# Kernel tuning notes

Measured on AMD Instinct MI355X. Metric: run time of the kernel, lower is better.

## Reference

```python
import jax, jax.numpy as jnp
from jax import lax
import numpy as np

EPS = 1e-5

def _conv(x, w, b, pad, dil=1):
    y = lax.conv_general_dilated(x, w, (1, 1), [(pad, pad), (pad, pad)],
                                 rhs_dilation=(dil, dil),
                                 dimension_numbers=('NCHW', 'OIHW', 'NCHW'))
    return y + b[None, :, None, None]

def _bn(x, g, b):
    # BatchNorm2d in training mode: batch stats over (N,H,W)
    m = x.mean((0, 2, 3), keepdims=True)
    v = x.var((0, 2, 3), keepdims=True)
    return (x - m) * lax.rsqrt(v + EPS) * g[None, :, None, None] + b[None, :, None, None]

def _median_filter(x, k=5):
    # faithful to source: 5x5 box SUM of reflect-padded shifts, then median over channels
    p = k // 2
    xp = jnp.pad(x, ((0, 0), (0, 0), (p, p), (p, p)), mode='reflect')
    s = lax.reduce_window(xp, 0.0, lax.add, (1, 1, k, k), (1, 1, 1, 1), 'VALID')
    return jnp.median(s, axis=1, keepdims=True)

def _idwt2_haar(ca, ch, cv, cd):
    # pywt.idwt2 haar convention: cH = row-detail ('da'), cV = col-detail ('ad')
    B, C, H, W = ca.shape
    y00 = (ca + ch + cv + cd) * 0.5
    y01 = (ca + ch - cv - cd) * 0.5
    y10 = (ca - ch + cv - cd) * 0.5
    y11 = (ca - ch - cv + cd) * 0.5
    even = jnp.stack([y00, y01], axis=-1).reshape(B, C, H, 2 * W)
    odd = jnp.stack([y10, y11], axis=-1).reshape(B, C, H, 2 * W)
    return jnp.stack([even, odd], axis=-2).reshape(B, C, 2 * H, 2 * W)

def _forward(ll_freq, hl_freq, lh_freq, hh_freq, w_ll, w_hl, w_lh, w_hh,
             cc_w, cc_b, bnc_g, bnc_b, e1_w, e1_b, fe_w, fe_b, e2_w, e2_b,
             bne_g, bne_b, cr_w, cr_b, bnr_g, bnr_b,
             adj_w, adj_b, cll_w, cll_b, chh_w, chh_b,
             c1_w, c1_b, c3_w, c3_b, c5_w, c5_b):
    C = hh_freq.shape[1]
    ll = w_ll * ll_freq
    hl = w_hl * hl_freq
    lh = w_lh * lh_freq
    hh = w_hh * hh_freq
    hh_m = jnp.tile(_median_filter(hh), (1, C, 1, 1))
    hh_l1 = hh_m + hh_freq
    # CCFEA SE-style block on concat(hl, lh)
    x = jnp.concatenate([hl, lh], axis=1)
    orig = x
    x = _conv(x, cc_w, cc_b, 0)
    x = _conv(x, e1_w, e1_b, 1)
    x = jax.nn.relu(_bn(x, bnc_g, bnc_b))
    x = _conv(x, fe_w, fe_b, 0)
    x = _conv(x, e2_w, e2_b, 2)
    x = jax.nn.relu(_bn(x, bne_g, bne_b))
    x = _conv(x, cr_w, cr_b, 0)
    x = _bn(x, bnr_g, bnr_b)
    x = orig * jax.nn.sigmoid(x)
    hl_l1, lh_l1 = jnp.split(x, 2, axis=1)
    # multi-kernel LL branch
    ll_l1 = _conv(ll, c1_w, c1_b, 1)
    ll_l1 = _conv(ll_l1, c3_w, c3_b, 2)
    ll_l1 = _conv(ll_l1, c5_w, c5_b, 3)
    ll_l2 = _conv(jnp.concatenate([ll_l1, ll], axis=1), adj_w, adj_b, 0)
    hl_l2 = _conv(jnp.concatenate([hl_l1, hl_freq], axis=1), adj_w, adj_b, 0)
    lh_l2 = _conv(jnp.concatenate([lh_l1, lh_freq], axis=1), adj_w, adj_b, 0)
    hh_a = jax.nn.leaky_relu(_conv(hh_l1, chh_w, chh_b, 0), 0.1)
    hh_l2 = jnp.tanh(_conv(hh_a, cll_w, cll_b, 4, dil=2))  # k=5, dilation=2, pad=4 -> same size
    return _idwt2_haar(ll_l2, hl_l2, lh_l2, hh_l2)

def setup_inputs() -> dict:
    key = jax.random.key(0)
    ks = jax.random.split(key, 16)
    B, C, H, W = 8, 64, 64, 64
    RED, EXP = 16, 8 * C  # reduction_ratio=16, expanded = (2C)*4 = 512
    f32 = jnp.float32
    def w(k, shape, s=0.05):
        return jax.random.normal(k, shape, dtype=f32) * s
    z = lambda n: jnp.zeros((n,), f32)
    o = lambda n: jnp.ones((n,), f32)
    return {
        'll_freq': jax.random.normal(ks[0], (B, C, H, W), dtype=f32),
        'hl_freq': jax.random.normal(ks[1], (B, C, H, W), dtype=f32),
        'lh_freq': jax.random.normal(ks[2], (B, C, H, W), dtype=f32),
        'hh_freq': jax.random.normal(ks[3], (B, C, H, W), dtype=f32),
        'w_ll': jnp.asarray(1.0, f32), 'w_hl': jnp.asarray(1.0, f32),
        'w_lh': jnp.asarray(1.0, f32), 'w_hh': jnp.asarray(1.0, f32),
        'cc_w': w(ks[4], (RED, 2 * C, 1, 1)), 'cc_b': z(RED),
        'bnc_g': o(RED), 'bnc_b': z(RED),
        'e1_w': w(ks[5], (RED, RED, 3, 3)), 'e1_b': z(RED),
        'fe_w': w(ks[6], (EXP, RED, 1, 1)), 'fe_b': z(EXP),
        'e2_w': w(ks[7], (EXP, EXP, 5, 5)), 'e2_b': z(EXP),
        'bne_g': o(EXP), 'bne_b': z(EXP),
        'cr_w': w(ks[8], (2 * C, EXP, 1, 1)), 'cr_b': z(2 * C),
        'bnr_g': o(2 * C), 'bnr_b': z(2 * C),
        'adj_w': w(ks[9], (C, 2 * C, 1, 1)), 'adj_b': z(C),
        'cll_w': w(ks[10], (C, C, 5, 5)), 'cll_b': z(C),
        'chh_w': w(ks[11], (C, C, 1, 1)), 'chh_b': z(C),
        'c1_w': w(ks[12], (C, C, 3, 3)), 'c1_b': z(C),
        'c3_w': w(ks[13], (C, C, 5, 5)), 'c3_b': z(C),
        'c5_w': w(ks[14], (C, C, 7, 7)), 'c5_b': z(C),
    }

def reference(ll_freq, hl_freq, lh_freq, hh_freq, w_ll, w_hl, w_lh, w_hh,
              cc_w, cc_b, bnc_g, bnc_b, e1_w, e1_b, fe_w, fe_b, e2_w, e2_b,
              bne_g, bne_b, cr_w, cr_b, bnr_g, bnr_b,
              adj_w, adj_b, cll_w, cll_b, chh_w, chh_b,
              c1_w, c1_b, c3_w, c3_b, c5_w, c5_b):
    return _forward(ll_freq, hl_freq, lh_freq, hh_freq, w_ll, w_hl, w_lh, w_hh,
                    cc_w, cc_b, bnc_g, bnc_b, e1_w, e1_b, fe_w, fe_b, e2_w, e2_b,
                    bne_g, bne_b, cr_w, cr_b, bnr_g, bnr_b,
                    adj_w, adj_b, cll_w, cll_b, chh_w, chh_b,
                    c1_w, c1_b, c3_w, c3_b, c5_w, c5_b)
```

## Files before the change

### kernel.cpp

```cpp
#include <hip/hip_runtime.h>
#include <math.h>


#define HWP 4096

typedef __attribute__((ext_vector_type(8))) short bf16x8;
typedef __attribute__((ext_vector_type(4))) float f32x4;

__device__ __forceinline__ unsigned short f2bf(float x) {
  unsigned int u = __float_as_uint(x);
  unsigned int r = (u + 0x7fffu + ((u >> 16) & 1u)) >> 16;
  return (unsigned short)r;
}
__device__ __forceinline__ float bf2f(unsigned short h) {
  return __uint_as_float(((unsigned int)h) << 16);
}

__device__ __forceinline__ void gload16(const void* g, void* l) {
  __builtin_amdgcn_global_load_lds(
      (const __attribute__((address_space(1))) unsigned int*)g,
      (__attribute__((address_space(3))) unsigned int*)l, 16, 0, 0);
}

__global__ void finalize_k(const float* __restrict__ s,
// ... 174 lines not shown
    __syncthreads();
  }
  if (out_mode >= 2) {
#pragma unroll
    for (int j = 0; j < 8; ++j) {
      int co = co0 + cog * 8 + j;
      float bs = bias[co];
      float r[2] = {acc0[j] + bs, acc1[j] + bs};
#pragma unroll
      for (int e = 0; e < 2; ++e) {
        float v = r[e];
        if (out_mode == 3) v = v < 0.f ? 0.1f * v : v;
        int px = pi * 2 + e;
        int w = px & 63;
        int slot = ((cog ^ ((w >> 1) & 3)) << 3) + j;
        int o = px * 32 + slot;
        unsigned short hsh = f2bf(v);
        sOH[o] = (short)hsh;
        if (o_lo) sOL[o] = (short)f2bf(v - bf2f(hsh));
      }
    }
    __syncthreads();
    int cb = co0 >> 5;
    size_t base = (size_t)(b * (COUT >> 5) + cb) * 131072 + (size_t)p0 * 32;
    for (int k = tid; k < 512; k += 256) {
      *(float4*)(o_hi + base + (size_t)k * 8) = *(float4*)&sOH[k * 8];
      if (o_lo)
        *(float4*)(o_lo + base + (size_t)k * 8) = *(float4*)&sOL[k * 8];
    }
  } else {
#pragma unroll
    for (int j = 0; j < 8; ++j) {
      int co = co0 + cog * 8 + j;
      if (co < COUT) {
        float bs = bias[co];
        float r0 = acc0[j] + bs;
        float r1 = acc1[j] + bs;
        if (out_mode == 1) {
          r0 = r0 < 0.f ? 0.1f * r0 : r0;
          r1 = r1 < 0.f ? 0.1f * r1 : r1;
        }
        float2 rr = make_float2(r0, r1);
        *(float2*)&out[(((size_t)(b * COUT + co)) << 12) + p0 + pi * 2] = rr;
      }
    }
  }
}

__global__ void __launch_bounds__(256) pack_k(
    const float* __restrict__ in, const float* __restrict__ scale_ptr,
    unsigned short* __restrict__ o_hi, unsigned short* __restrict__ o_lo) {
  __shared__ float lds[32][130];
  int bx = blockIdx.x;
  int pc = bx & 31, cb = (bx >> 5) & 1, b = bx >> 6;
  int p0 = pc * 128;
  float sc = scale_ptr ? scale_ptr[0] : 1.f;
  int tid = threadIdx.x;
  for (int i = tid; i < 4096; i += 256) {
    int c = i >> 7, px = i & 127;
    lds[c][px] = in[((size_t)(b * 64 + cb * 32 + c) << 12) + p0 + px] * sc;
  }
  __syncthreads();
  size_t base = (size_t)(b * 2 + cb) * 131072 + (size_t)p0 * 32;
  for (int k = tid; k < 512; k += 256) {
    int p = k >> 2, gsw = k & 3;
    int w = p & 63;
    int g = gsw ^ ((w >> 1) & 3);
    bf16x8 hi, lo;
#pragma unroll
    for (int j = 0; j < 8; ++j) {
      float v = lds[g * 8 + j][p];
      unsigned short h = f2bf(v);
      hi[j] = (short)h;
      lo[j] = (short)f2bf(v - bf2f(h));
    }
    *(bf16x8*)(o_hi + base + (size_t)k * 8) = hi;
    *(bf16x8*)(o_lo + base + (size_t)k * 8) = lo;
  }
}

__device__ __forceinline__ void ws_body(const float* __restrict__ w,
                                        unsigned short* __restrict__ Wt,
                                        int bx, int CIN, int KK) {
  int cbci = bx / KK, tap = bx - cbci * KK;
  unsigned short* dst = Wt + (size_t)bx * 2048;
  for (int d = threadIdx.x; d < 2048; d += 256) {
    int co = d >> 5, s = d & 31;
    int g = (s >> 3) ^ ((co >> 1) & 3);
    int cil = (g << 3) + (s & 7);
    dst[d] = f2bf(w[(size_t)(co * CIN + cbci * 32 + cil) * KK + tap]);
  }
}

__global__ void __launch_bounds__(256) prep_all_k(
    const float* __restrict__ e2w, const float* __restrict__ crw,
    const float* __restrict__ c1w, const float* __restrict__ c3w,
    const float* __restrict__ c5w, const float* __restrict__ cllw,
    const float* __restrict__ adjw, unsigned short* __restrict__ Wt,
    unsigned short* __restrict__ Wcr, unsigned short* __restrict__ Wc1,
    unsigned short* __restrict__ Wc3, unsigned short* __restrict__ Wc5,
    unsigned short* __restrict__ Wcll, unsigned short* __restrict__ Wadj,
    float* __restrict__ SM) {
  __shared__ short lw[32][800];
  int bx = blockIdx.x, tid = threadIdx.x;
  if (bx < 256) {
    int cbco = bx >> 6, cbci = (bx >> 2) & 15, cog = bx & 3;
    const float* src =
        e2w + ((size_t)(cbco * 128 + cog * 32) * 512 + cbci * 32) * 25;
    for (int i = tid; i < 25600; i += 256) {
      int co_l = i / 800, r = i - co_l * 800;
      lw[co_l][r] = (short)f2bf(src[(size_t)co_l * 12800 + r]);
    }
    __syncthreads();
    unsigned short* dstb =
        Wt + (((size_t)((cbco * 16 + cbci) * 25)) << 12) + cog * 1024;
    for (int k = tid; k < 6400; k += 256) {
      int tap = k >> 8, d4 = (k & 255) << 2;
      short4 o;
      short* op = (short*)&o;
#pragma unroll
      for (int u = 0; u < 4; ++u) {
        int d = d4 + u;
        int col = d >> 5, s = d & 31;
        int g = (s >> 3) ^ ((col >> 1) & 3);
        int cil = (g << 3) + (s & 7);
        op[u] = lw[col][cil * 25 + tap];
      }
      *(short4*)(dstb + (size_t)tap * 4096 + d4) = o;
    }
  } else if (bx < 272) {
    int cb = bx - 256;
    unsigned short* dst = Wcr + (size_t)cb * 4096;
    for (int d = tid; d < 4096; d += 256) {
      int co = d >> 5, s = d & 31;
      int g = (s >> 3) ^ ((co >> 1) & 3);
      int cil = (g << 3) + (s & 7);
      dst[d] = f2bf(crw[(size_t)co * 512 + cb * 32 + cil]);
    }
  } else if (bx < 290) {
    ws_body(c1w, Wc1, bx - 272, 64, 9);
  } else if (bx < 340) {
    ws_body(c3w, Wc3, bx - 290, 64, 25);
  } else if (bx < 438) {
    ws_body(c5w, Wc5, bx - 340, 64, 49);
  } else if (bx < 488) {
    ws_body(cllw, Wcll, bx - 438, 64, 25);
  } else if (bx < 492) {
    ws_body(adjw, Wadj, bx - 488, 128, 1);
  } else {
    for (int i = tid; i < 1280; i += 256) SM[i] = 0.f;
  }
}

__global__ void __launch_bounds__(256, 3) e2_mfma_k(
    const unsigned short* __restrict__ y4h, const unsigned short* __restrict__ Wt,
    const float* __restrict__ bias, unsigned short* __restrict__ E2h,
    float* __restrict__ sum5, float* __restrict__ sq5) {
  __shared__ __align__(16) char smem[43008];
  const int tid = threadIdx.x;
  const int lane = tid & 63;
  const int wid = tid >> 6;
  int logical = ((blockIdx.x & 7) << 7) + (blockIdx.x >> 3);
  int cbco = logical >> 8;
  int rem = logical & 255;
  int rowpair = rem >> 3;
  int b = rem & 7;
  int h0 = rowpair << 1;
  const int wm = wid >> 1, wn = wid & 1;
  const int l15 = lane & 15, lg = lane >> 4;

  int colterm[4][5];
#pragma unroll
  for (int mi = 0; mi < 4; ++mi)
#pragma unroll
    for (int kw = 0; kw < 5; ++kw) {
      int col = mi * 16 + l15 + kw;
      colterm[mi][kw] = col * 64 + ((lg ^ (((col + 62) >> 1) & 3)) << 4);
    }
  int bterm[4];
#pragma unroll
  for (int ni = 0; ni < 4; ++ni) {
    int c = wn * 64 + ni * 16 + l15;
    bterm[ni] = c * 64 + ((lg ^ ((c >> 1) & 3)) << 4);
  }

  if (tid < 96) {
    int g = tid & 3, e = tid >> 2;
    int s = e >> 2, cp = e & 3;
    int col = (cp < 2) ? cp : (64 + cp);
    *(float4*)(smem + s * 4352 + col * 64 + g * 16) =
        make_float4(0.f, 0.f, 0.f, 0.f);
  }

  f32x4 acc[4][4];
#pragma unroll
  for (int i = 0; i < 4; ++i)
#pragma unroll
    for (int j = 0; j < 4; ++j) acc[i][j] = (f32x4)(0.f);

#pragma unroll 1
  for (int cb = 0; cb < 16; ++cb) {
#pragma unroll
    for (int s = 0; s < 6; ++s) {
      int irow = h0 - 2 + s;
      char* ldsrow = smem + s * 4352 + 128;
      if ((unsigned)irow < 64u) {
        const unsigned short* src =
            y4h + (((size_t)(b * 16 + cb) * 64 + irow) << 11);
        gload16(src + (wid << 9) + (lane << 3), ldsrow + (wid << 10));
      } else {
        *(float4*)(ldsrow + (wid << 10) + (lane << 4)) =
            make_float4(0.f, 0.f, 0.f, 0.f);
      }
    }
    {
      const unsigned short* src = Wt + ((size_t)((cbco * 16 + cb) * 25) << 12);
#pragma unroll
      for (int k = 0; k < 2; ++k) {
        int c2 = wid * 2 + k;
        gload16(src + (c2 << 9) + (lane << 3), smem + 26624 + (c2 << 10));
      }
    }
    __syncthreads();

#pragma unroll 1
    for (int kh = 0; kh < 5; ++kh) {
      int abase = (wm + kh) * 4352;
#pragma unroll
      for (int kw = 0; kw < 5; ++kw) {
        int tap = kh * 5 + kw;
        if (tap < 24) {
          const unsigned short* src =
              Wt + ((size_t)((cbco * 16 + cb) * 25 + tap + 1) << 12);
          int buf = (tap + 1) & 1;
#pragma unroll
          for (int k = 0; k < 2; ++k) {
            int c2 = wid * 2 + k;
            gload16(src + (c2 << 9) + (lane << 3),
                    smem + 26624 + (buf << 13) + (c2 << 10));
          }
        }
        char* bbase = smem + 26624 + ((tap & 1) << 13);
        bf16x8 bfr[4];
#pragma unroll
        for (int ni = 0; ni < 4; ++ni)
          bfr[ni] = *(bf16x8*)(bbase + bterm[ni]);
#pragma unroll
        for (int mi = 0; mi < 4; ++mi) {
          bf16x8 ah = *(bf16x8*)(smem + abase + colterm[mi][kw]);
#pragma unroll
          for (int ni = 0; ni < 4; ++ni) {
            acc[mi][ni] = __builtin_amdgcn_mfma_f32_16x16x32_bf16(
                ah, bfr[ni], acc[mi][ni], 0, 0, 0);
          }
        }
        __syncthreads();
      }
    }
  }

  short* H = (short*)smem;
#pragma unroll
  for (int ni = 0; ni < 4; ++ni) {
    int co_l = wn * 64 + ni * 16 + l15;
    int cb_l = co_l >> 5, ch = co_l & 31;
    float bs = bias[cbco * 128 + co_l];
    float ps = 0.f, pq = 0.f;
#pragma unroll
    for (int mi = 0; mi < 4; ++mi) {
#pragma unroll
      for (int j = 0; j < 4; ++j) {
        int w = mi * 16 + lg * 4 + j;
        float v = acc[mi][ni][j] + bs;
        ps += v;
        pq += v * v;
        int slot = (((ch >> 3) ^ ((w >> 1) & 3)) << 3) + (ch & 7);
        H[(cb_l * 128 + wm * 64 + w) * 32 + slot] = (short)f2bf(v);
      }
    }
    ps += __shfl_xor(ps, 16, 64); ps += __shfl_xor(ps, 32, 64);
    pq += __shfl_xor(pq, 16, 64); pq += __shfl_xor(pq, 32, 64);
    if (lg == 0) {
      atomicAdd(&sum5[cbco * 128 + co_l], ps);
      atomicAdd(&sq5[cbco * 128 + co_l], pq);
    }
  }
  __syncthreads();
  for (int k = tid; k < 2048; k += 256) {
    int cb_l = k >> 9, r = k & 511;
    size_t gb = ((size_t)(b * 16 + cbco * 4 + cb_l) * 4096 + h0 * 64) * 32 +
                (size_t)r * 8;
    *(float4*)(E2h + gb) = *(float4*)(H + cb_l * 4096 + r * 8);
  }
}

__global__ void __launch_bounds__(256, 2) cr_mfma_k(
    const unsigned short* __restrict__ E2h, const unsigned short* __restrict__ Wcr,
    const float* __restrict__ ab2, const float* __restrict__ bias,
    float* __restrict__ y7, float* __restrict__ sum3, float* __restrict__ sq3) {
  __shared__ __align__(16) char smem[20480];
  float* sa = (float*)(smem + 16384);
  float* sb = sa + 512;
  const int tid = threadIdx.x;
  const int lane = tid & 63;
  const int wid = tid >> 6;
  const int b = blockIdx.y;
  const int p0 = blockIdx.x << 6;
  const int wm = wid >> 1, wn = wid & 1;
  const int l15 = lane & 15, lg = lane >> 4;

  for (int i = tid; i < 512; i += 256) {
    sa[i] = ab2[i];
    sb[i] = ab2[512 + i];
  }

  int aterm[2];
#pragma unroll
  for (int mi = 0; mi < 2; ++mi) {
    int px = wm * 32 + mi * 16 + l15;
    aterm[mi] = px * 64 + ((lg ^ ((px >> 1) & 3)) << 4);
  }
  int bterm[4];
#pragma unroll
  for (int ni = 0; ni < 4; ++ni) {
    int c = wn * 64 + ni * 16 + l15;
    bterm[ni] = c * 64 + ((lg ^ ((c >> 1) & 3)) << 4);
  }

  f32x4 acc[2][4];
#pragma unroll
  for (int i = 0; i < 2; ++i)
#pragma unroll
    for (int j = 0; j < 4; ++j) acc[i][j] = (f32x4)(0.f);

  const int spx = tid >> 2, sgs = tid & 3;
  const int sg = sgs ^ ((spx >> 1) & 3);
  __syncthreads();

#pragma unroll 1
  for (int cb = 0; cb < 16; ++cb) {
    {
      size_t src = ((size_t)(b * 16 + cb) * 4096 + p0 + spx) * 32 + sgs * 8;
      bf16x8 h8 = *(const bf16x8*)(E2h + src);
      bf16x8 oh, ol;
      int cib = cb * 32 + sg * 8;
#pragma unroll
      for (int j = 0; j < 8; ++j) {
        float x = bf2f((unsigned short)h8[j]);
        float v = fmaxf(sa[cib + j] * x + sb[cib + j], 0.f);
        unsigned short hh2 = f2bf(v);
        oh[j] = (short)hh2;
        ol[j] = (short)f2bf(v - bf2f(hh2));
      }
      *(bf16x8*)(smem + spx * 64 + sgs * 16) = oh;
      *(bf16x8*)(smem + 4096 + spx * 64 + sgs * 16) = ol;
    }
    {
      const unsigned short* srcB = Wcr + (size_t)cb * 4096;
#pragma unroll
      for (int k = 0; k < 2; ++k) {
        int c2 = wid * 2 + k;
        gload16(srcB + (c2 << 9) + (lane << 3), smem + 8192 + (c2 << 10));
      }
    }
    __syncthreads();
    bf16x8 bfr[4];
#pragma unroll
    for (int ni = 0; ni < 4; ++ni)
      bfr[ni] = *(bf16x8*)(smem + 8192 + bterm[ni]);
#pragma unroll
    for (int mi = 0; mi < 2; ++mi) {
      bf16x8 ah = *(bf16x8*)(smem + aterm[mi]);
      bf16x8 al = *(bf16x8*)(smem + 4096 + aterm[mi]);
#pragma unroll
      for (int ni = 0; ni < 4; ++ni) {
        acc[mi][ni] = __builtin_amdgcn_mfma_f32_16x16x32_bf16(
            ah, bfr[ni], acc[mi][ni], 0, 0, 0);
        acc[mi][ni] = __builtin_amdgcn_mfma_f32_16x16x32_bf16(
            al, bfr[ni], acc[mi][ni], 0, 0, 0);
      }
    }
    __syncthreads();
  }

#pragma unroll
  for (int ni = 0; ni < 4; ++ni) {
    int co = wn * 64 + ni * 16 + l15;
    float bs = bias[co];
    float ps = 0.f, pq = 0.f;
#pragma unroll
    for (int mi = 0; mi < 2; ++mi) {
      f32x4 v = acc[mi][ni];
      v += (f32x4)(bs);
#pragma unroll
      for (int j = 0; j < 4; ++j) { ps += v[j]; pq += v[j] * v[j]; }
      int px = p0 + wm * 32 + mi * 16 + lg * 4;
      *(f32x4*)(y7 + (((size_t)(b * 128 + co)) << 12) + px) = v;
    }
    ps += __shfl_xor(ps, 16, 64); ps += __shfl_xor(ps, 32, 64);
    pq += __shfl_xor(pq, 16, 64); pq += __shfl_xor(pq, 32, 64);
    if (lg == 0) {
      atomicAdd(&sum3[co], ps);
      atomicAdd(&sq3[co], pq);
    }
  }
}

__global__ void __launch_bounds__(256) adj_mfma_k(
    const float* __restrict__ ll_a, const float* __restrict__ ll_freq,
    const float* __restrict__ hl_freq, const float* __restrict__ lh_freq,
    const float* __restrict__ y7, const float* __restrict__ ab3,
    const float* __restrict__ w_ll, const float* __restrict__ w_hl,
    const float* __restrict__ w_lh, const unsigned short* __restrict__ Wadj,
    const float* __restrict__ bias, float* __restrict__ ll_l2,
    float* __restrict__ hl_l2, float* __restrict__ lh_l2) {
  __shared__ __align__(16) char smem[20480];
  const int tid = threadIdx.x;
  const int lane = tid & 63;
  const int wid = tid >> 6;
  const int p0 = (int)blockIdx.x << 7;
  const int var = blockIdx.y;
  const int b = blockIdx.z;
  const int wm = wid >> 1, wn = wid & 1;
  const int l15 = lane & 15, lg = lane >> 4;

  int aterm[4];
#pragma unroll
  for (int mi = 0; mi < 4; ++mi) {
    int px = wm * 64 + mi * 16 + l15;
    aterm[mi] = px * 64 + ((lg ^ ((px >> 1) & 3)) << 4);
  }
  int bterm[2];
#pragma unroll
  for (int ni = 0; ni < 2; ++ni) {
    int c = wn * 32 + ni * 16 + l15;
    bterm[ni] = c * 64 + ((lg ^ ((c >> 1) & 3)) << 4);
  }

  f32x4 acc[4][2];
#pragma unroll
  for (int i = 0; i < 4; ++i)
#pragma unroll
    for (int j = 0; j < 2; ++j) acc[i][j] = (f32x4)(0.f);

  const float* fr = (var == 1) ? hl_freq : lh_freq;
  float scl = (var == 0) ? w_ll[0] : ((var == 1) ? w_hl[0] : w_lh[0]);

#pragma unroll 1
  for (int cb = 0; cb < 4; ++cb) {
#pragma unroll 1
    for (int pass = 0; pass < 16; ++pass) {
      int ci = pass * 2 + (tid >> 7);
      int px = tid & 127;
      int c = cb * 32 + ci;
      int p = p0 + px;
      float v;
      if (var == 0) {
        v = (c < 64) ? ll_a[(((size_t)(b * 64 + c)) << 12) + p]
                     : scl * ll_freq[(((size_t)(b * 64 + c - 64)) << 12) + p];
      } else {
        if (c < 64) {
          int yc = (var == 1) ? c : (64 + c);
          float arg = ab3[yc] * y7[(((size_t)(b * 128 + yc)) << 12) + p] +
                      ab3[128 + yc];
          float sg = 1.f / (1.f + expf(-arg));
          v = scl * fr[(((size_t)(b * 64 + c)) << 12) + p] * sg;
        } else {
          v = fr[(((size_t)(b * 64 + c - 64)) << 12) + p];
        }
      }
      unsigned short h = f2bf(v);
      int gs = (ci >> 3) ^ ((px >> 1) & 3);
      int off = px * 64 + gs * 16 + (ci & 7) * 2;
      *(short*)(smem + off) = (short)h;
      *(short*)(smem + 8192 + off) = (short)f2bf(v - bf2f(h));
    }
    gload16(Wadj + (size_t)cb * 2048 + (tid << 3), smem + 16384 + (tid << 4));
    __syncthreads();
    bf16x8 bfr[2];
#pragma unroll
    for (int ni = 0; ni < 2; ++ni)
      bfr[ni] = *(bf16x8*)(smem + 16384 + bterm[ni]);
#pragma unroll
    for (int mi = 0; mi < 4; ++mi) {
      bf16x8 ah = *(bf16x8*)(smem + aterm[mi]);
      bf16x8 al = *(bf16x8*)(smem + 8192 + aterm[mi]);
#pragma unroll
      for (int ni = 0; ni < 2; ++ni) {
        acc[mi][ni] = __builtin_amdgcn_mfma_f32_16x16x32_bf16(
            ah, bfr[ni], acc[mi][ni], 0, 0, 0);
        acc[mi][ni] = __builtin_amdgcn_mfma_f32_16x16x32_bf16(
            al, bfr[ni], acc[mi][ni], 0, 0, 0);
      }
    }
    __syncthreads();
  }

  float* out = (var == 0) ? ll_l2 : ((var == 1) ? hl_l2 : lh_l2);
#pragma unroll
  for (int ni = 0; ni < 2; ++ni) {
    int co = wn * 32 + ni * 16 + l15;
    float bs = bias[co];
#pragma unroll
    for (int mi = 0; mi < 4; ++mi) {
      f32x4 v = acc[mi][ni];
      v += (f32x4)(bs);
      int px = p0 + wm * 64 + mi * 16 + lg * 4;
      *(f32x4*)(out + (((size_t)(b * 64 + co)) << 12) + px) = v;
    }
  }
}

template <int K, int DIL, int OUTMODE>
__global__ void __launch_bounds__(256, 2) convmf_k(
    const unsigned short* __restrict__ inh, const unsigned short* __restrict__ inl,
    const unsigned short* __restrict__ Wsm, const float* __restrict__ bias,
    float* __restrict__ out_f, unsigned short* __restrict__ o_hi,
    unsigned short* __restrict__ o_lo) {
  constexpr int PAD = (K - 1) / 2 * DIL;
  constexpr int ROWS = 2 + 2 * PAD;
  constexpr int CW = 64 + 2 * PAD;
  constexpr int RB = CW * 64;
  constexpr int ABYTES = ROWS * RB;
  constexpr int KK = K * K;
  __shared__ __align__(16) char smem[2 * ABYTES + 8192];
  const int tid = threadIdx.x;
  const int lane = tid & 63;
  const int wid = tid >> 6;
  const int b = blockIdx.x >> 5;
  const int h0 = (blockIdx.x & 31) << 1;
  const int wm = wid >> 1, wn = wid & 1;
  const int l15 = lane & 15, lg = lane >> 4;

  int colterm[4][K];
#pragma unroll
  for (int mi = 0; mi < 4; ++mi)
#pragma unroll
    for (int kw = 0; kw < K; ++kw) {
      int e = mi * 16 + l15 + kw * DIL;
      colterm[mi][kw] = e * 64 + ((lg ^ (((e - PAD + 64) >> 1) & 3)) << 4);
    }
  int bterm[2];
#pragma unroll
  for (int ni = 0; ni < 2; ++ni) {
    int c = wn * 32 + ni * 16 + l15;
    bterm[ni] = c * 64 + ((lg ^ ((c >> 1) & 3)) << 4);
  }

  for (int i = tid; i < 2 * ROWS * 2 * PAD * 4; i += 256) {
    int c4 = i & 3;
    int r1 = i >> 2;
    int e = r1 % (2 * PAD);
    int r2 = r1 / (2 * PAD);
    int r = r2 % ROWS;
    int part = r2 / ROWS;
    int col = (e < PAD) ? e : (e + 64);
    *(float4*)(smem + part * ABYTES + r * RB + col * 64 + c4 * 16) =
        make_float4(0.f, 0.f, 0.f, 0.f);
  }

  f32x4 acc[4][2];
#pragma unroll
  for (int i = 0; i < 4; ++i)
#pragma unroll
    for (int j = 0; j < 2; ++j) acc[i][j] = (f32x4)(0.f);

  const int part = wid >> 1;
  const int s0 = (wid & 1) * (ROWS / 2);
  const unsigned short* srcA = part ? inl : inh;

#pragma unroll 1
  for (int cb = 0; cb < 2; ++cb) {
#pragma unroll
    for (int si = 0; si < ROWS / 2; ++si) {
      int s = s0 + si;
      int irow = h0 - PAD + s;
      char* ldsrow = smem + part * ABYTES + s * RB + PAD * 64;
      if ((unsigned)irow < 64u) {
        const unsigned short* src =
            srcA + (((size_t)(b * 2 + cb) << 12) + (irow << 6)) * 32;
#pragma unroll
        for (int c = 0; c < 4; ++c)
          gload16(src + (c << 9) + (lane << 3), ldsrow + (c << 10));
      } else {
#pragma unroll
        for (int c = 0; c < 4; ++c)
          *(float4*)(ldsrow + (c << 10) + (lane << 4)) =
              make_float4(0.f, 0.f, 0.f, 0.f);
      }
    }
    {
      const unsigned short* srcB = Wsm + (size_t)(cb * KK) * 2048;
      gload16(srcB + (tid << 3), smem + 2 * ABYTES + (tid << 4));
    }
    __syncthreads();

#pragma unroll 1
    for (int kh = 0; kh < K; ++kh) {
      int abase = (wm + kh * DIL) * RB;
#pragma unroll
      for (int kw = 0; kw < K; ++kw) {
        int tap = kh * K + kw;
        if (tap + 1 < KK) {
          const unsigned short* srcB = Wsm + (size_t)(cb * KK + tap + 1) * 2048;
          gload16(srcB + (tid << 3),
                  smem + 2 * ABYTES + (((tap + 1) & 1) << 12) + (tid << 4));
        }
        char* bbase = smem + 2 * ABYTES + ((tap & 1) << 12);
        bf16x8 bfr[2];
#pragma unroll
        for (int ni = 0; ni < 2; ++ni)
          bfr[ni] = *(bf16x8*)(bbase + bterm[ni]);
#pragma unroll
        for (int mi = 0; mi < 4; ++mi) {
          bf16x8 ah = *(bf16x8*)(smem + abase + colterm[mi][kw]);
          bf16x8 al = *(bf16x8*)(smem + ABYTES + abase + colterm[mi][kw]);
#pragma unroll
          for (int ni = 0; ni < 2; ++ni) {
            acc[mi][ni] = __builtin_amdgcn_mfma_f32_16x16x32_bf16(
                ah, bfr[ni], acc[mi][ni], 0, 0, 0);
            acc[mi][ni] = __builtin_amdgcn_mfma_f32_16x16x32_bf16(
                al, bfr[ni], acc[mi][ni], 0, 0, 0);
          }
        }
        __syncthreads();
      }
    }
  }

  if (OUTMODE == 0) {
    short* soH = (short*)smem;
    short* soL = (short*)(smem + ABYTES);
#pragma unroll
    for (int mi = 0; mi < 4; ++mi)
#pragma unroll
      for (int ni = 0; ni < 2; ++ni) {
        int co = wn * 32 + ni * 16 + l15;
        float bs = bias[co];
        int ch = co & 31;
#pragma unroll
        for (int j = 0; j < 4; ++j) {
          int w = mi * 16 + lg * 4 + j;
          float v = acc[mi][ni][j] + bs;
          int slot = (((ch >> 3) ^ ((w >> 1) & 3)) << 3) + (ch & 7);
          int o = ((wm * 2 + wn) * 64 + w) * 32 + slot;
          unsigned short hsh = f2bf(v);
          soH[o] = (short)hsh;
          soL[o] = (short)f2bf(v - bf2f(hsh));
        }
      }
    __syncthreads();
    for (int k = tid; k < 1024; k += 256) {
      int grp = k >> 8;
      int row = grp >> 1, cbo = grp & 1;
      size_t dstb = (size_t)(b * 2 + cbo) * 131072 +
                    (size_t)((h0 + row) << 6) * 32 + (size_t)(k & 255) * 8;
      *(float4*)(o_hi + dstb) = *(float4*)(soH + k * 8);
      *(float4*)(o_lo + dstb) = *(float4*)(soL + k * 8);
    }
  } else {
    int row = h0 + wm;
#pragma unroll
    for (int ni = 0; ni < 2; ++ni) {
      int co = wn * 32 + ni * 16 + l15;
      float bs = bias[co];
#pragma unroll
      for (int mi = 0; mi < 4; ++mi) {
        int col = mi * 16 + lg * 4;
        f32x4 v = acc[mi][ni];
        v += (f32x4)(bs);
        if (OUTMODE == 2) {
#pragma unroll
          for (int j = 0; j < 4; ++j) v[j] = tanhf(v[j]);
        }
        *(f32x4*)(out_f + ((size_t)(b * 64 + co) * 64 + row) * 64 + col) = v;
      }
    }
  }
}

template <int K, int DIL, int CI_T, int OUTMODE>
__global__ void __launch_bounds__(256) convK_k(
    const float* __restrict__ in, const float* __restrict__ wgt,
    const float* __restrict__ bias, float* __restrict__ out, int CIN, int COUT,
    const float* __restrict__ scale_ptr) {
  constexpr int IH = 32 + (K - 1) * DIL;
  constexpr int IW = 32 + (K - 1) * DIL;
  constexpr int PAD = (K - 1) / 2 * DIL;
  constexpr int KK = K * K;
  __shared__ __align__(16) float s_in[CI_T][IH][IW];
  __shared__ __align__(16) float s_w[CI_T * KK * 16];
  int tid = threadIdx.x;
  int tx = tid & 15, ty = tid >> 4;
  int w0 = blockIdx.x * 32, h0 = blockIdx.y * 32;
  int ncog = COUT >> 4;
  int cog = blockIdx.z % ncog;
  int b = blockIdx.z / ncog;
  int co0 = cog << 4;
  float scale = scale_ptr ? scale_ptr[0] : 1.f;
  float a00[16] = {}, a01[16] = {}, a10[16] = {}, a11[16] = {};
  for (int ci0 = 0; ci0 < CIN; ci0 += CI_T) {
    for (int idx = tid; idx < CI_T * IH * IW; idx += 256) {
      int ci = idx / (IH * IW);
      int r = idx - ci * (IH * IW);
      int iy = r / IW;
      int ix = r - iy * IW;
      int gh = h0 - PAD + iy, gw = w0 - PAD + ix;
      float v = 0.f;
      if ((unsigned)gh < 64u && (unsigned)gw < 64u)
        v = in[((((size_t)(b * CIN + ci0 + ci)) << 6) + (size_t)gh << 6) + gw] * scale;
      s_in[ci][iy][ix] = v;
    }
    for (int idx = tid; idx < CI_T * KK * 16; idx += 256) {
      int co = idx & 15;
      int t = (idx >> 4) % KK;
      int ci = (idx >> 4) / KK;
      s_w[(ci * KK + t) * 16 + co] =
          wgt[((size_t)(co0 + co) * CIN + ci0 + ci) * KK + t];
    }
    __syncthreads();
    for (int ci = 0; ci < CI_T; ++ci) {
#pragma unroll
      for (int t = 0; t < KK; ++t) {
        int kh = t / K, kw = t - (t / K) * K;
        int iy = ty * 2 + kh * DIL, ix = tx * 2 + kw * DIL;
        float v00 = s_in[ci][iy][ix];
        float v01 = s_in[ci][iy][ix + 1];
        float v10 = s_in[ci][iy + 1][ix];
        float v11 = s_in[ci][iy + 1][ix + 1];
        const float4* wp = (const float4*)&s_w[(ci * KK + t) * 16];
#pragma unroll
        for (int q = 0; q < 4; ++q) {
          float4 wv = wp[q];
          float wj[4] = {wv.x, wv.y, wv.z, wv.w};
#pragma unroll
          for (int r = 0; r < 4; ++r) {
            a00[q * 4 + r] += v00 * wj[r];
            a01[q * 4 + r] += v01 * wj[r];
            a10[q * 4 + r] += v10 * wj[r];
            a11[q * 4 + r] += v11 * wj[r];
          }
        }
      }
    }
    __syncthreads();
  }
  int oh = h0 + ty * 2, ow = w0 + tx * 2;
#pragma unroll
  for (int j = 0; j < 16; ++j) {
    int co = co0 + j;
    float bs = bias[co];
    float r00 = a00[j] + bs, r01 = a01[j] + bs;
    float r10 = a10[j] + bs, r11 = a11[j] + bs;
    if (OUTMODE == 1) {
      r00 = tanhf(r00); r01 = tanhf(r01);
      r10 = tanhf(r10); r11 = tanhf(r11);
    }
    size_t ob = ((((size_t)(b * COUT + co)) << 6) + (size_t)oh) << 6;
    *(float2*)&out[ob + ow] = make_float2(r00, r01);
    *(float2*)&out[ob + 64 + ow] = make_float2(r10, r11);
  }
}

__global__ void __launch_bounds__(256) idwt_k(
    const float* __restrict__ ca, const float* __restrict__ ch,
    const float* __restrict__ cv, const float* __restrict__ cd,
    float* __restrict__ out) {
  int i = blockIdx.x * 256 + threadIdx.x;
  float A = ca[i], Hd = ch[i], V = cv[i], D = cd[i];
  float y00 = (A + Hd + V + D) * 0.5f;
  float y01 = (A + Hd - V - D) * 0.5f;
  float y10 = (A - Hd + V - D) * 0.5f;
  float y11 = (A - Hd - V + D) * 0.5f;
  int w = i & 63;
  int h = (i >> 6) & 63;
  int bc = i >> 12;
  size_t ob = (((size_t)bc * 128) + 2 * h) * 128 + 2 * w;
  *(float2*)&out[ob] = make_float2(y00, y01);
  *(float2*)&out[ob + 128] = make_float2(y10, y11);
}

extern "C" void kernel_launch(void* const* d_in, const int* in_sizes, int n_in,
                              void* d_out, int out_size, void* d_ws,
                              size_t ws_size, hipStream_t stream) {
  const float* ll_freq = (const float*)d_in[0];
  const float* hl_freq = (const float*)d_in[1];
  const float* lh_freq = (const float*)d_in[2];
  const float* hh_freq = (const float*)d_in[3];
  const float* w_ll = (const float*)d_in[4];
  const float* w_hl = (const float*)d_in[5];
  const float* w_lh = (const float*)d_in[6];
  const float* w_hh = (const float*)d_in[7];
  const float* cc_w = (const float*)d_in[8];
  const float* cc_b = (const float*)d_in[9];
  const float* bnc_g = (const float*)d_in[10];
  const float* bnc_b = (const float*)d_in[11];
  const float* e1_w = (const float*)d_in[12];
  const float* e1_b = (const float*)d_in[13];
  const float* fe_w = (const float*)d_in[14];
  const float* fe_b = (const float*)d_in[15];
  const float* e2_w = (const float*)d_in[16];
  const float* e2_b = (const float*)d_in[17];
  const float* bne_g = (const float*)d_in[18];
  const float* bne_b = (const float*)d_in[19];
  const float* cr_w = (const float*)d_in[20];
  const float* cr_b = (const float*)d_in[21];
  const float* bnr_g = (const float*)d_in[22];
  const float* bnr_b = (const float*)d_in[23];
  const float* adj_w = (const float*)d_in[24];
  const float* adj_b = (const float*)d_in[25];
  const float* cll_w = (const float*)d_in[26];
  const float* cll_b = (const float*)d_in[27];
  const float* chh_w = (const float*)d_in[28];
  const float* chh_b = (const float*)d_in[29];
  const float* c1_w = (const float*)d_in[30];
  const float* c1_b = (const float*)d_in[31];
  const float* c3_w = (const float*)d_in[32];
  const float* c3_b = (const float*)d_in[33];
  const float* c5_w = (const float*)d_in[34];
  const float* c5_b = (const float*)d_in[35];

  const size_t MB = 1ull << 20;
  char* ws = (char*)d_ws;
  unsigned short* y4h = (unsigned short*)(ws);
  float* regA = (float*)(ws);
  unsigned short* E2h = (unsigned short*)(ws + 64 * MB);
  float* y7   = (float*)(ws + 128 * MB);
  float* y1   = (float*)(ws + 144 * MB);
  float* y2   = (float*)(ws + 146 * MB);
  unsigned short* Wt = (unsigned short*)(ws + 148 * MB);
  char* base162 = ws + 162 * MB;
  float* hh_m = (float*)(base162);
  float* st1  = (float*)(base162 + 128 * 1024);
  float* SM   = (float*)(base162 + 132 * 1024);
  float* AB2  = (float*)(base162 + 140 * 1024);
  float* AB3  = (float*)(base162 + 146 * 1024);
  unsigned short* Wc1  = (unsigned short*)(base162 + 256 * 1024);
  unsigned short* Wc3  = (unsigned short*)(base162 + 512 * 1024);
  unsigned short* Wc5  = (unsigned short*)(base162 + 768 * 1024);
  unsigned short* Wcll = (unsigned short*)(base162 + 1280 * 1024);
  unsigned short* Wcr  = (unsigned short*)(base162 + 1536 * 1024);
  unsigned short* Wadj = (unsigned short*)(base162 + 1664 * 1024);
  float* s512 = SM;
  float* q512 = SM + 512;
  float* s128 = SM + 1024;
  float* q128 = SM + 1152;

  const size_t F2M = 2097152;
  float* ll_a  = regA + 0 * F2M;
  float* ll_l2 = regA + 1 * F2M;
  float* hl_l2 = regA + 2 * F2M;
  float* lh_l2 = regA + 3 * F2M;
  unsigned short* Ph = (unsigned short*)(ws + 48 * MB);
  unsigned short* Pl = (unsigned short*)(ws + 52 * MB);
  unsigned short* Qh = (unsigned short*)(ws + 56 * MB);
  unsigned short* Ql = (unsigned short*)(ws + 60 * MB);
  float* S = (float*)(ws + 64 * MB);
  float* hh_l2 = (float*)(ws + 64 * MB);

  dim3 blk(256);

  prep_all_k<<<dim3(493), blk, 0, stream>>>(e2_w, cr_w, c1_w, c3_w, c5_w,
                                            cll_w, adj_w, Wt, Wcr, Wc1, Wc3,
                                            Wc5, Wcll, Wadj, SM);

  boxsum_k<<<dim3(512), blk, 0, stream>>>(hh_freq, w_hh, S);
  med_k<<<dim3(512), blk, 0, stream>>>(S, hh_m);

  conv1x1_k<<<dim3(32, 1, 8), blk, 0, stream>>>(
      hl_freq, lh_freq, 64, w_hl, w_lh, nullptr, nullptr, nullptr, nullptr, 1,
      cc_w, cc_b, y1, 128, 16, 0, nullptr, nullptr);

  convK_k<3, 1, 8, 0><<<dim3(2, 2, 8), blk, 0, stream>>>(y1, e1_w, e1_b, y2, 16,
                                                         16, nullptr);
  stats_k<<<dim3(16), blk, 0, stream>>>(y2, st1, 16, 8);

  conv1x1_k<<<dim3(32, 16, 8), blk, 0, stream>>>(
      y2, nullptr, 0, nullptr, nullptr, st1, bnc_g, bnc_b, nullptr, 2, fe_w,
      fe_b, nullptr, 16, 512, 2, y4h, nullptr);

  e2_mfma_k<<<dim3(1024), blk, 0, stream>>>(y4h, Wt, e2_b, E2h, s512, q512);
  finalize_k<<<dim3(1), dim3(512), 0, stream>>>(s512, q512, bne_g, bne_b,
                                                1.f / 32768.f, 512, AB2);

  cr_mfma_k<<<dim3(64, 8), blk, 0, stream>>>(E2h, Wcr, AB2, cr_b, y7, s128,
                                             q128);
  finalize_k<<<dim3(1), dim3(128), 0, stream>>>(s128, q128, bnr_g, bnr_b,
                                                1.f / 32768.f, 128, AB3);

  pack_k<<<dim3(512), blk, 0, stream>>>(ll_freq, w_ll, Ph, Pl);
  convmf_k<3, 1, 0><<<dim3(256), blk, 0, stream>>>(Ph, Pl, Wc1, c1_b, nullptr,
                                                   Qh, Ql);
  convmf_k<5, 1, 0><<<dim3(256), blk, 0, stream>>>(Qh, Ql, Wc3, c3_b, nullptr,
                                                   Ph, Pl);
  convmf_k<7, 1, 1><<<dim3(256), blk, 0, stream>>>(Ph, Pl, Wc5, c5_b, ll_a,
                                                   nullptr, nullptr);

  adj_mfma_k<<<dim3(32, 3, 8), blk, 0, stream>>>(
      ll_a, ll_freq, hl_freq, lh_freq, y7, AB3, w_ll, w_hl, w_lh, Wadj, adj_b,
      ll_l2, hl_l2, lh_l2);

  conv1x1_k<<<dim3(32, 2, 8), blk, 0, stream>>>(
      hh_freq, nullptr, 0, nullptr, nullptr, nullptr, nullptr, nullptr, hh_m, 3,
      chh_w, chh_b, nullptr, 64, 64, 3, Qh, Ql);

  convmf_k<5, 2, 2><<<dim3(256), blk, 0, stream>>>(Qh, Ql, Wcll, cll_b, hh_l2,
                                                   nullptr, nullptr);

  idwt_k<<<dim3(8192), blk, 0, stream>>>(ll_l2, hl_l2, lh_l2, hh_l2,
                                         (float*)d_out);
}
```

Before: 989.6 us.

## Retile e2 conv, drop bf16 hi/lo split in cr/adj/cll, stream conv weights

The e2 5x5 conv kernel now computes four output rows per block across all 128 output channels with an 8-wide accumulator tile, halving the grid and doubling reuse of each weight tap. The cr, adj and final cll convolutions drop the second low-order bf16 pass, so they run single bf16 MFMAs and use less LDS. convmf_k now reads weights straight from global memory into registers with a one-tap prefetch, which removes the LDS weight double buffer and the per-tap barrier. The cost is lower numerical precision in several convolutions, more register pressure in e2, and a two-pass epilogue to write out the results.

After: 925.5 us. 6.5% less time.

```diff
diff --git a/kernel.cpp b/kernel.cpp
--- a/kernel.cpp
+++ b/kernel.cpp
@@ -350,21 +350,21 @@
   }
 }
 
-__global__ void __launch_bounds__(256, 3) e2_mfma_k(
+__global__ void __launch_bounds__(256, 2) e2_mfma_k(
     const unsigned short* __restrict__ y4h, const unsigned short* __restrict__ Wt,
     const float* __restrict__ bias, unsigned short* __restrict__ E2h,
     float* __restrict__ sum5, float* __restrict__ sq5) {
-  __shared__ __align__(16) char smem[43008];
+  __shared__ __align__(16) char smem[51200];
   const int tid = threadIdx.x;
   const int lane = tid & 63;
   const int wid = tid >> 6;
-  int logical = ((blockIdx.x & 7) << 7) + (blockIdx.x >> 3);
-  int cbco = logical >> 8;
-  int rem = logical & 255;
-  int rowpair = rem >> 3;
+  int logical = ((blockIdx.x & 7) << 6) + (blockIdx.x >> 3);
+  int cbco = logical >> 7;
+  int rem = logical & 127;
+  int rowgroup = rem >> 3;
   int b = rem & 7;
-  int h0 = rowpair << 1;
-  const int wm = wid >> 1, wn = wid & 1;
+  int h0 = rowgroup << 2;
+  const int wm = wid;
   const int l15 = lane & 15, lg = lane >> 4;
 
   int colterm[4][5];
@@ -375,14 +375,14 @@
       int col = mi * 16 + l15 + kw;
       colterm[mi][kw] = col * 64 + ((lg ^ (((col + 62) >> 1) & 3)) << 4);
     }
-  int bterm[4];
-#pragma unroll
-  for (int ni = 0; ni < 4; ++ni) {
-    int c = wn * 64 + ni * 16 + l15;
+  int bterm[8];
+#pragma unroll
+  for (int ni = 0; ni < 8; ++ni) {
+    int c = ni * 16 + l15;
     bterm[ni] = c * 64 + ((lg ^ ((c >> 1) & 3)) << 4);
   }
 
-  if (tid < 96) {
+  if (tid < 128) {
     int g = tid & 3, e = tid >> 2;
     int s = e >> 2, cp = e & 3;
     int col = (cp < 2) ? cp : (64 + cp);
@@ -390,25 +390,31 @@
         make_float4(0.f, 0.f, 0.f, 0.f);
   }
 
-  f32x4 acc[4][4];
+  f32x4 acc[4][8];
 #pragma unroll
   for (int i = 0; i < 4; ++i)
 #pragma unroll
-    for (int j = 0; j < 4; ++j) acc[i][j] = (f32x4)(0.f);
+    for (int j = 0; j < 8; ++j) acc[i][j] = (f32x4)(0.f);
 
 #pragma unroll 1
   for (int cb = 0; cb < 16; ++cb) {
-#pragma unroll
-    for (int s = 0; s < 6; ++s) {
+    __syncthreads();
+#pragma unroll
+    for (int si = 0; si < 2; ++si) {
+      int s = wid + si * 4;
       int irow = h0 - 2 + s;
       char* ldsrow = smem + s * 4352 + 128;
       if ((unsigned)irow < 64u) {
         const unsigned short* src =
             y4h + (((size_t)(b * 16 + cb) * 64 + irow) << 11);
-        gload16(src + (wid << 9) + (lane << 3), ldsrow + (wid << 10));
+#pragma unroll
+        for (int c = 0; c < 4; ++c)
+          gload16(src + (c << 9) + (lane << 3), ldsrow + (c << 10));
       } else {
-        *(float4*)(ldsrow + (wid << 10) + (lane << 4)) =
-            make_float4(0.f, 0.f, 0.f, 0.f);
+#pragma unroll
+        for (int c = 0; c < 4; ++c)
+          *(float4*)(ldsrow + (c << 10) + (lane << 4)) =
+              make_float4(0.f, 0.f, 0.f, 0.f);
       }
     }
     {
@@ -416,7 +422,7 @@
 #pragma unroll
       for (int k = 0; k < 2; ++k) {
         int c2 = wid * 2 + k;
-        gload16(src + (c2 << 9) + (lane << 3), smem + 26624 + (c2 << 10));
+        gload16(src + (c2 << 9) + (lane << 3), smem + 34816 + (c2 << 10));
       }
     }
     __syncthreads();
@@ -435,19 +441,19 @@
           for (int k = 0; k < 2; ++k) {
             int c2 = wid * 2 + k;
             gload16(src + (c2 << 9) + (lane << 3),
-                    smem + 26624 + (buf << 13) + (c2 << 10));
+                    smem + 34816 + (buf << 13) + (c2 << 10));
           }
         }
-        char* bbase = smem + 26624 + ((tap & 1) << 13);
-        bf16x8 bfr[4];
-#pragma unroll
-        for (int ni = 0; ni < 4; ++ni)
+        char* bbase = smem + 34816 + ((tap & 1) << 13);
+        bf16x8 bfr[8];
+#pragma unroll
+        for (int ni = 0; ni < 8; ++ni)
           bfr[ni] = *(bf16x8*)(bbase + bterm[ni]);
 #pragma unroll
         for (int mi = 0; mi < 4; ++mi) {
           bf16x8 ah = *(bf16x8*)(smem + abase + colterm[mi][kw]);
 #pragma unroll
-          for (int ni = 0; ni < 4; ++ni) {
+          for (int ni = 0; ni < 8; ++ni) {
             acc[mi][ni] = __builtin_amdgcn_mfma_f32_16x16x32_bf16(
                 ah, bfr[ni], acc[mi][ni], 0, 0, 0);
           }
@@ -457,25 +463,19 @@
     }
   }
 
-  short* H = (short*)smem;
-#pragma unroll
-  for (int ni = 0; ni < 4; ++ni) {
-    int co_l = wn * 64 + ni * 16 + l15;
-    int cb_l = co_l >> 5, ch = co_l & 31;
+#pragma unroll
+  for (int ni = 0; ni < 8; ++ni) {
+    int co_l = ni * 16 + l15;
     float bs = bias[cbco * 128 + co_l];
     float ps = 0.f, pq = 0.f;
 #pragma unroll
-    for (int mi = 0; mi < 4; ++mi) {
+    for (int mi = 0; mi < 4; ++mi)
 #pragma unroll
       for (int j = 0; j < 4; ++j) {
-        int w = mi * 16 + lg * 4 + j;
         float v = acc[mi][ni][j] + bs;
         ps += v;
         pq += v * v;
-        int slot = (((ch >> 3) ^ ((w >> 1) & 3)) << 3) + (ch & 7);
-        H[(cb_l * 128 + wm * 64 + w) * 32 + slot] = (short)f2bf(v);
-      }
-    }
+      }
     ps += __shfl_xor(ps, 16, 64); ps += __shfl_xor(ps, 32, 64);
     pq += __shfl_xor(pq, 16, 64); pq += __shfl_xor(pq, 32, 64);
     if (lg == 0) {
@@ -483,12 +483,38 @@
       atomicAdd(&sq5[cbco * 128 + co_l], pq);
     }
   }
-  __syncthreads();
-  for (int k = tid; k < 2048; k += 256) {
-    int cb_l = k >> 9, r = k & 511;
-    size_t gb = ((size_t)(b * 16 + cbco * 4 + cb_l) * 4096 + h0 * 64) * 32 +
-                (size_t)r * 8;
-    *(float4*)(E2h + gb) = *(float4*)(H + cb_l * 4096 + r * 8);
+
+  short* H = (short*)smem;
+#pragma unroll 1
+  for (int pass = 0; pass < 2; ++pass) {
+    if ((wid >> 1) == pass) {
+      int r_l = wid & 1;
+#pragma unroll
+      for (int ni = 0; ni < 8; ++ni) {
+        int co_l = ni * 16 + l15;
+        int cb_l = co_l >> 5, ch = co_l & 31;
+        float bs = bias[cbco * 128 + co_l];
+#pragma unroll
+        for (int mi = 0; mi < 4; ++mi)
+#pragma unroll
+          for (int j = 0; j < 4; ++j) {
+            int w = mi * 16 + lg * 4 + j;
+            float v = acc[mi][ni][j] + bs;
+            int slot = (((ch >> 3) ^ ((w >> 1) & 3)) << 3) + (ch & 7);
+            H[(cb_l * 128 + r_l * 64 + w) * 32 + slot] = (short)f2bf(v);
+          }
+      }
+    }
+    __syncthreads();
+    for (int k = tid; k < 2048; k += 256) {
+      int cb_l = k >> 9, r = k & 511;
+      size_t gb =
+          ((size_t)(b * 16 + cbco * 4 + cb_l) * 4096 + (h0 + 2 * pass) * 64) *
+              32 +
+          (size_t)r * 8;
+      *(float4*)(E2h + gb) = *(float4*)(H + cb_l * 4096 + r * 8);
+    }
+    __syncthreads();
   }
 }
 
@@ -496,8 +522,8 @@
     const unsigned short* __restrict__ E2h, const unsigned short* __restrict__ Wcr,
     const float* __restrict__ ab2, const float* __restrict__ bias,
     float* __restrict__ y7, float* __restrict__ sum3, float* __restrict__ sq3) {
-  __shared__ __align__(16) char smem[20480];
-  float* sa = (float*)(smem + 16384);
+  __shared__ __align__(16) char smem[16384];
+  float* sa = (float*)(smem + 12288);
   float* sb = sa + 512;
   const int tid = threadIdx.x;
   const int lane = tid & 63;
@@ -540,42 +566,36 @@
     {
       size_t src = ((size_t)(b * 16 + cb) * 4096 + p0 + spx) * 32 + sgs * 8;
       bf16x8 h8 = *(const bf16x8*)(E2h + src);
-      bf16x8 oh, ol;
+      bf16x8 oh;
       int cib = cb * 32 + sg * 8;
 #pragma unroll
       for (int j = 0; j < 8; ++j) {
         float x = bf2f((unsigned short)h8[j]);
         float v = fmaxf(sa[cib + j] * x + sb[cib + j], 0.f);
-        unsigned short hh2 = f2bf(v);
-        oh[j] = (short)hh2;
-        ol[j] = (short)f2bf(v - bf2f(hh2));
+        oh[j] = (short)f2bf(v);
       }
       *(bf16x8*)(smem + spx * 64 + sgs * 16) = oh;
-      *(bf16x8*)(smem + 4096 + spx * 64 + sgs * 16) = ol;
     }
     {
       const unsigned short* srcB = Wcr + (size_t)cb * 4096;
 #pragma unroll
       for (int k = 0; k < 2; ++k) {
         int c2 = wid * 2 + k;
-        gload16(srcB + (c2 << 9) + (lane << 3), smem + 8192 + (c2 << 10));
+        gload16(srcB + (c2 << 9) + (lane << 3), smem + 4096 + (c2 << 10));
       }
     }
     __syncthreads();
     bf16x8 bfr[4];
 #pragma unroll
     for (int ni = 0; ni < 4; ++ni)
-      bfr[ni] = *(bf16x8*)(smem + 8192 + bterm[ni]);
+      bfr[ni] = *(bf16x8*)(smem + 4096 + bterm[ni]);
 #pragma unroll
     for (int mi = 0; mi < 2; ++mi) {
       bf16x8 ah = *(bf16x8*)(smem + aterm[mi]);
-      bf16x8 al = *(bf16x8*)(smem + 4096 + aterm[mi]);
 #pragma unroll
       for (int ni = 0; ni < 4; ++ni) {
         acc[mi][ni] = __builtin_amdgcn_mfma_f32_16x16x32_bf16(
             ah, bfr[ni], acc[mi][ni], 0, 0, 0);
-        acc[mi][ni] = __builtin_amdgcn_mfma_f32_16x16x32_bf16(
-            al, bfr[ni], acc[mi][ni], 0, 0, 0);
       }
     }
     __syncthreads();
@@ -612,7 +632,7 @@
     const float* __restrict__ w_lh, const unsigned short* __restrict__ Wadj,
     const float* __restrict__ bias, float* __restrict__ ll_l2,
     float* __restrict__ hl_l2, float* __restrict__ lh_l2) {
-  __shared__ __align__(16) char smem[20480];
+  __shared__ __align__(16) char smem[12288];
   const int tid = threadIdx.x;
   const int lane = tid & 63;
   const int wid = tid >> 6;
@@ -667,28 +687,23 @@
           v = fr[(((size_t)(b * 64 + c - 64)) << 12) + p];
         }
       }
-      unsigned short h = f2bf(v);
       int gs = (ci >> 3) ^ ((px >> 1) & 3);
       int off = px * 64 + gs * 16 + (ci & 7) * 2;
-      *(short*)(smem + off) = (short)h;
-      *(short*)(smem + 8192 + off) = (short)f2bf(v - bf2f(h));
-    }
-    gload16(Wadj + (size_t)cb * 2048 + (tid << 3), smem + 16384 + (tid << 4));
+      *(short*)(smem + off) = (short)f2bf(v);
+    }
+    gload16(Wadj + (size_t)cb * 2048 + (tid << 3), smem + 8192 + (tid << 4));
     __syncthreads();
     bf16x8 bfr[2];
 #pragma unroll
     for (int ni = 0; ni < 2; ++ni)
-      bfr[ni] = *(bf16x8*)(smem + 16384 + bterm[ni]);
+      bfr[ni] = *(bf16x8*)(smem + 8192 + bterm[ni]);
 #pragma unroll
     for (int mi = 0; mi < 4; ++mi) {
       bf16x8 ah = *(bf16x8*)(smem + aterm[mi]);
-      bf16x8 al = *(bf16x8*)(smem + 8192 + aterm[mi]);
 #pragma unroll
       for (int ni = 0; ni < 2; ++ni) {
         acc[mi][ni] = __builtin_amdgcn_mfma_f32_16x16x32_bf16(
             ah, bfr[ni], acc[mi][ni], 0, 0, 0);
-        acc[mi][ni] = __builtin_amdgcn_mfma_f32_16x16x32_bf16(
-            al, bfr[ni], acc[mi][ni], 0, 0, 0);
       }
     }
     __syncthreads();
@@ -709,7 +724,7 @@
   }
 }
 
-template <int K, int DIL, int OUTMODE>
+template <int K, int DIL, int OUTMODE, int LO>
 __global__ void __launch_bounds__(256, 2) convmf_k(
     const unsigned short* __restrict__ inh, const unsigned short* __restrict__ inl,
     const unsigned short* __restrict__ Wsm, const float* __restrict__ bias,
@@ -721,7 +736,8 @@
   constexpr int RB = CW * 64;
   constexpr int ABYTES = ROWS * RB;
   constexpr int KK = K * K;
-  __shared__ __align__(16) char smem[2 * ABYTES + 8192];
+  constexpr int SBYTES = LO ? 2 * ABYTES : ABYTES;
+  __shared__ __align__(16) char smem[SBYTES];
   const int tid = threadIdx.x;
   const int lane = tid & 63;
   const int wid = tid >> 6;
@@ -745,7 +761,7 @@
     bterm[ni] = c * 64 + ((lg ^ ((c >> 1) & 3)) << 4);
   }
 
-  for (int i = tid; i < 2 * ROWS * 2 * PAD * 4; i += 256) {
+  for (int i = tid; i < (LO ? 2 : 1) * ROWS * 2 * PAD * 4; i += 256) {
     int c4 = i & 3;
     int r1 = i >> 2;
     int e = r1 % (2 * PAD);
@@ -763,70 +779,90 @@
 #pragma unroll
     for (int j = 0; j < 2; ++j) acc[i][j] = (f32x4)(0.f);
 
-  const int part = wid >> 1;
-  const int s0 = (wid & 1) * (ROWS / 2);
-  const unsigned short* srcA = part ? inl : inh;
-
 #pragma unroll 1
   for (int cb = 0; cb < 2; ++cb) {
-#pragma unroll
-    for (int si = 0; si < ROWS / 2; ++si) {
-      int s = s0 + si;
-      int irow = h0 - PAD + s;
-      char* ldsrow = smem + part * ABYTES + s * RB + PAD * 64;
-      if ((unsigned)irow < 64u) {
-        const unsigned short* src =
-            srcA + (((size_t)(b * 2 + cb) << 12) + (irow << 6)) * 32;
-#pragma unroll
-        for (int c = 0; c < 4; ++c)
-          gload16(src + (c << 9) + (lane << 3), ldsrow + (c << 10));
-      } else {
-#pragma unroll
-        for (int c = 0; c < 4; ++c)
-          *(float4*)(ldsrow + (c << 10) + (lane << 4)) =
-              make_float4(0.f, 0.f, 0.f, 0.f);
-      }
-    }
-    {
-      const unsigned short* srcB = Wsm + (size_t)(cb * KK) * 2048;
-      gload16(srcB + (tid << 3), smem + 2 * ABYTES + (tid << 4));
-    }
-    __syncthreads();
-
+    __syncthreads();
+    if (LO) {
+      const int part = wid >> 1;
+      const int s0 = (wid & 1) * (ROWS / 2);
+      const unsigned short* srcA = part ? inl : inh;
+#pragma unroll
+      for (int si = 0; si < ROWS / 2; ++si) {
+        int s = s0 + si;
+        int irow = h0 - PAD + s;
+        char* ldsrow = smem + part * ABYTES + s * RB + PAD * 64;
+        if ((unsigned)irow < 64u) {
+          const unsigned short* src =
+              srcA + (((size_t)(b * 2 + cb) << 12) + (irow << 6)) * 32;
+#pragma unroll
+          for (int c = 0; c < 4; ++c)
+            gload16(src + (c << 9) + (lane << 3), ldsrow + (c << 10));
+        } else {
+#pragma unroll
+          for (int c = 0; c < 4; ++c)
+            *(float4*)(ldsrow + (c << 10) + (lane << 4)) =
+                make_float4(0.f, 0.f, 0.f, 0.f);
+        }
+      }
+    } else {
+      for (int s = wid; s < ROWS; s += 4) {
+        int irow = h0 - PAD + s;
+        char* ldsrow = smem + s * RB + PAD * 64;
+        if ((unsigned)irow < 64u) {
+          const unsigned short* src =
+              inh + (((size_t)(b * 2 + cb) << 12) + (irow << 6)) * 32;
+#pragma unroll
+          for (int c = 0; c < 4; ++c)
+            gload16(src + (c << 9) + (lane << 3), ldsrow + (c << 10));
+        } else {
+#pragma unroll
+          for (int c = 0; c < 4; ++c)
+            *(float4*)(ldsrow + (c << 10) + (lane << 4)) =
+                make_float4(0.f, 0.f, 0.f, 0.f);
+        }
+      }
+    }
+    __syncthreads();
+
+    const char* WB0 = (const char*)Wsm + (size_t)(cb * KK) * 4096;
+    bf16x8 bc0 = *(const bf16x8*)(WB0 + bterm[0]);
+    bf16x8 bc1 = *(const bf16x8*)(WB0 + bterm[1]);
 #pragma unroll 1
     for (int kh = 0; kh < K; ++kh) {
       int abase = (wm + kh * DIL) * RB;
 #pragma unroll
       for (int kw = 0; kw < K; ++kw) {
         int tap = kh * K + kw;
+        bf16x8 bn0 = bc0, bn1 = bc1;
         if (tap + 1 < KK) {
-          const unsigned short* srcB = Wsm + (size_t)(cb * KK + tap + 1) * 2048;
-          gload16(srcB + (tid << 3),
-                  smem + 2 * ABYTES + (((tap + 1) & 1) << 12) + (tid << 4));
-        }
-        char* bbase = smem + 2 * ABYTES + ((tap & 1) << 12);
-        bf16x8 bfr[2];
-#pragma unroll
-        for (int ni = 0; ni < 2; ++ni)
-          bfr[ni] = *(bf16x8*)(bbase + bterm[ni]);
+          const char* WB =
+              (const char*)Wsm + (size_t)(cb * KK + tap + 1) * 4096;
+          bn0 = *(const bf16x8*)(WB + bterm[0]);
+          bn1 = *(const bf16x8*)(WB + bterm[1]);
+        }
 #pragma unroll
         for (int mi = 0; mi < 4; ++mi) {
           bf16x8 ah = *(bf16x8*)(smem + abase + colterm[mi][kw]);
-          bf16x8 al = *(bf16x8*)(smem + ABYTES + abase + colterm[mi][kw]);
-#pragma unroll
-          for (int ni = 0; ni < 2; ++ni) {
-            acc[mi][ni] = __builtin_amdgcn_mfma_f32_16x16x32_bf16(
-                ah, bfr[ni], acc[mi][ni], 0, 0, 0);
-            acc[mi][ni] = __builtin_amdgcn_mfma_f32_16x16x32_bf16(
-                al, bfr[ni], acc[mi][ni], 0, 0, 0);
+          acc[mi][0] = __builtin_amdgcn_mfma_f32_16x16x32_bf16(ah, bc0,
+                                                              acc[mi][0], 0, 0, 0);
+          acc[mi][1] = __builtin_amdgcn_mfma_f32_16x16x32_bf16(ah, bc1,
+                                                              acc[mi][1], 0, 0, 0);
+          if (LO) {
+            bf16x8 al = *(bf16x8*)(smem + ABYTES + abase + colterm[mi][kw]);
+            acc[mi][0] = __builtin_amdgcn_mfma_f32_16x16x32_bf16(
+                al, bc0, acc[mi][0], 0, 0, 0);
+            acc[mi][1] = __builtin_amdgcn_mfma_f32_16x16x32_bf16(
+                al, bc1, acc[mi][1], 0, 0, 0);
           }
         }
-        __syncthreads();
+        bc0 = bn0;
+        bc1 = bn1;
       }
     }
   }
 
   if (OUTMODE == 0) {
+    __syncthreads();
     short* soH = (short*)smem;
     short* soL = (short*)(smem + ABYTES);
 #pragma unroll
@@ -1077,7 +1113,7 @@
       y2, nullptr, 0, nullptr, nullptr, st1, bnc_g, bnc_b, nullptr, 2, fe_w,
       fe_b, nullptr, 16, 512, 2, y4h, nullptr);
 
-  e2_mfma_k<<<dim3(1024), blk, 0, stream>>>(y4h, Wt, e2_b, E2h, s512, q512);
+  e2_mfma_k<<<dim3(512), blk, 0, stream>>>(y4h, Wt, e2_b, E2h, s512, q512);
   finalize_k<<<dim3(1), dim3(512), 0, stream>>>(s512, q512, bne_g, bne_b,
                                                 1.f / 32768.f, 512, AB2);
 
@@ -1087,12 +1123,12 @@
                                                 1.f / 32768.f, 128, AB3);
 
   pack_k<<<dim3(512), blk, 0, stream>>>(ll_freq, w_ll, Ph, Pl);
-  convmf_k<3, 1, 0><<<dim3(256), blk, 0, stream>>>(Ph, Pl, Wc1, c1_b, nullptr,
-                                                   Qh, Ql);
-  convmf_k<5, 1, 0><<<dim3(256), blk, 0, stream>>>(Qh, Ql, Wc3, c3_b, nullptr,
-                                                   Ph, Pl);
-  convmf_k<7, 1, 1><<<dim3(256), blk, 0, stream>>>(Ph, Pl, Wc5, c5_b, ll_a,
-                                                   nullptr, nullptr);
+  convmf_k<3, 1, 0, 1><<<dim3(256), blk, 0, stream>>>(Ph, Pl, Wc1, c1_b,
+                                                      nullptr, Qh, Ql);
+  convmf_k<5, 1, 0, 1><<<dim3(256), blk, 0, stream>>>(Qh, Ql, Wc3, c3_b,
+                                                      nullptr, Ph, Pl);
+  convmf_k<7, 1, 1, 1><<<dim3(256), blk, 0, stream>>>(Ph, Pl, Wc5, c5_b, ll_a,
+                                                      nullptr, nullptr);
 
   adj_mfma_k<<<dim3(32, 3, 8), blk, 0, stream>>>(
       ll_a, ll_freq, hl_freq, lh_freq, y7, AB3, w_ll, w_hl, w_lh, Wadj, adj_b,
@@ -1100,10 +1136,10 @@
 
   conv1x1_k<<<dim3(32, 2, 8), blk, 0, stream>>>(
       hh_freq, nullptr, 0, nullptr, nullptr, nullptr, nullptr, nullptr, hh_m, 3,
-      chh_w, chh_b, nullptr, 64, 64, 3, Qh, Ql);
-
-  convmf_k<5, 2, 2><<<dim3(256), blk, 0, stream>>>(Qh, Ql, Wcll, cll_b, hh_l2,
-                                                   nullptr, nullptr);
+      chh_w, chh_b, nullptr, 64, 64, 3, Qh, nullptr);
+
+  convmf_k<5, 2, 2, 0><<<dim3(256), blk, 0, stream>>>(Qh, nullptr, Wcll, cll_b,
+                                                      hh_l2, nullptr, nullptr);
 
   idwt_k<<<dim3(8192), blk, 0, stream>>>(ll_l2, hl_l2, lh_l2, hh_l2,
                                          (float*)d_out);
```
